# Kernel optimization log

Measured on AMD Instinct MI355X. Metric: run time of the kernel, lower is better.

The kernel has to match this reference:

```python
import jax, jax.numpy as jnp
import numpy as np

B = 128
IN = 256
NLVL = 6
KLVL = 3
CH = 4
C = 4 * CH * CH          # 64 channels per node
OU = 8                   # out_filter_siz_u
OV = 8                   # out_filter_siz_v
NK = 2 ** KLVL           # 8 leaf nodes per axis
W_SCALE = 1.0 / 16.0     # ~1/sqrt(2*2*C) so 7 stacked relu-convs stay numerically sane


def setup_inputs() -> dict:
    key = jax.random.key(0)
    ks = jax.random.split(key, 2 * NLVL + 4)
    fx = IN // 2 ** NLVL  # 4: input patch filter size
    inp = {}
    inp["in_data"] = jax.random.normal(ks[0], (B, IN, IN, 1), jnp.float32)
    inp["in_filter"] = jax.random.normal(ks[1], (fx, fx, 1, C), jnp.float32) * W_SCALE
    inp["in_bias"] = jnp.zeros((C,), jnp.float32)
    i = 2
    for lvl in range(1, NLVL + 1):
        n = 2 ** min(lvl, KLVL)  # node grid: grows to 2^klvl then stays
        inp[f"f{lvl}"] = jax.random.normal(ks[i], (n, n, 2, 2, C, C), jnp.float32) * W_SCALE
        inp[f"b{lvl}"] = jnp.zeros((n, n, C), jnp.float32)
        i += 1
    inp["Wd"] = jax.random.normal(ks[i], (NK, NK, 2, C, OU * OV), jnp.float32) * W_SCALE
    return inp


def _node_conv(x, w, b):
    # x: [Nu,Nv,B,H,W,C]; w: [Nu,Nv,2,2,C,C]; 2x2 stride-2 VALID conv per node
    Nu, Nv, Bn, H, W, Cc = x.shape
    xr = x.reshape(Nu, Nv, Bn, H // 2, 2, W // 2, 2, Cc)
    y = jnp.einsum('uvbhxwyc,uvxyco->uvbhwo', xr, w)
    return jax.nn.relu(y + b[:, :, None, None, None, :])


def _forward(in_data, in_filter, in_bias, fs, bs, Wd):
    Bn = in_data.shape[0]
    fx, fy = in_filter.shape[0], in_filter.shape[1]
    # input interp conv: stride == kernel -> non-overlapping patch GEMM
    xr = in_data[..., 0].reshape(Bn, in_data.shape[1] // fx, fx, in_data.shape[2] // fy, fy)
    x = jax.nn.relu(jnp.einsum('bxpyq,pqc->bxyc', xr, in_filter[:, :, 0, :]) + in_bias)
    x = x[None, None]  # [1,1,B,2^nlvl,2^nlvl,C] node grid
    for lvl in range(1, NLVL + 1):
        if lvl <= KLVL:
            # children (itu,itv) read parent (itu//2, itv//2)
            x = jnp.repeat(jnp.repeat(x, 2, axis=0), 2, axis=1)
        x = _node_conv(x, fs[lvl - 1], bs[lvl - 1])
    feats = x[:, :, :, 0, 0, :]  # [NK,NK,B,C]; spatial is 1x1 at level nlvl
    out = jnp.einsum('uvbc,uvrck->uvbrk', feats, Wd)  # r in {real, imag}
    out = out.reshape(NK, NK, Bn, 2, OU, OV)
    out = jnp.transpose(out, (2, 0, 4, 1, 5, 3))  # [B,itu,ou,itv,ov,2]
    return out.reshape(Bn, NK * OU, NK * OV, 2)


def reference(in_data, in_filter, in_bias, f1, b1, f2, b2, f3, b3, f4, b4, f5, b5, f6, b6, Wd):
    fs = (f1, f2, f3, f4, f5, f6)
    bs = (b1, b2, b3, b4, b5, b6)
    return _forward(in_data, in_filter, in_bias, fs, bs, Wd)
```

## Files before the change

### kernel.cpp

```cpp
#include <hip/hip_runtime.h>
#include <hip/hip_bf16.h>
#include <cstdint>
#include <cstddef>


typedef __attribute__((ext_vector_type(8))) short short8;
typedef __attribute__((ext_vector_type(4))) float f32x4;
typedef unsigned short ushort_t;

static __device__ __forceinline__ float b2f(const __hip_bfloat16 x) {
    return __bfloat162float(x);
}
static __device__ __forceinline__ ushort_t f2bf(float x) {
    __hip_bfloat16 h = __float2bfloat16(x);
    ushort_t u;
    __builtin_memcpy(&u, &h, 2);
    return u;
}
static __device__ __forceinline__ void gl_lds16(const void* g, void* l) {
    __builtin_amdgcn_global_load_lds(
        (const __attribute__((address_space(1))) void*)g,
        (__attribute__((address_space(3))) void*)l, 16, 0, 0);
}
#define WAIT_LGKM0() __builtin_amdgcn_s_waitcnt(0xC07F)
#define WAIT_VM0()   __builtin_amdgcn_s_waitcnt(0x0F70)

#define PREP_BLOCKS 2533

static __device__ __forceinline__ void prep_work(
    int gid, int isbf,
    const void* f1, const void* f2, const void* f3,
    const void* f4, const void* f5, const void* f6, const void* wdsrc,
    const void* b1, const void* b2, const void* b3,
    const void* b4, const void* b5, const void* b6,
    ushort_t* __restrict__ wbuf, ushort_t* __restrict__ wdbuf,
    float* __restrict__ bbuf)
{
    if (gid >= 648448) return;
    if (gid >= 630784) {
        const int bg = gid - 630784;
        const void* src; int base;
        if      (bg <   256) { src = b1; base = 0;     }
        else if (bg <  1280) { src = b2; base = 256;   }
        else if (bg <  5376) { src = b3; base = 1280;  }
        else if (bg <  9472) { src = b4; base = 5376;  }
        else if (bg < 13568) { src = b5; base = 9472;  }
        else                 { src = b6; base = 13568; }
        const int local = bg - base;
        bbuf[bg] = isbf ? b2f(((const __hip_bfloat16*)src)[local])
                        : ((const float*)src)[local];
        return;
    }
    if (gid >= 565248) {
        const int local = gid - 565248;
        const int lane = local & 63;
        const int slot = (local >> 6) & 15;
        const int site = local >> 10;
        const int ks2 = slot >> 3, nh = slot & 7, q = lane >> 4;
        const int n = nh * 16 + (lane & 15);
        const int r = n >> 6, kk = n & 63;
        const int cbase = ks2 * 32 + q * 8;
        ushort_t pk[8];
        if (isbf) {
            const ushort_t* s = (const ushort_t*)wdsrc;
            #pragma unroll
            for (int j = 0; j < 8; j++)
                pk[j] = s[(((size_t)(site * 2 + r) * 64 + cbase + j) * 64) + kk];
        } else {
            const float* s = (const float*)wdsrc;
            #pragma unroll
            for (int j = 0; j < 8; j++)
                pk[j] = f2bf(s[(((size_t)(site * 2 + r) * 64 + cbase + j) * 64) + kk]);
        }
        *(uint4*)&wdbuf[(size_t)local * 8] = *(uint4*)pk;
        return;
    }
    const void* fsrc; int base;
    if      (gid <   8192) { fsrc = f1; base = 0;      }
    else if (gid <  40960) { fsrc = f2; base = 8192;   }
    else if (gid < 172032) { fsrc = f3; base = 40960;  }
    else if (gid < 303104) { fsrc = f4; base = 172032; }
    else if (gid < 434176) { fsrc = f5; base = 303104; }
    else                   { fsrc = f6; base = 434176; }
    const int local = gid - base;
    const int lane = local & 63;
    const int slot = (local >> 6) & 7;
    const int sitetap = local >> 9;
    const int ks = slot >> 2, nh = slot & 3, q = lane >> 4;
    const int n = (lane & 15) + nh * 16;
    const int kbase = ks * 32 + q * 8;
    ushort_t pk[8];
    if (isbf) {
        const ushort_t* s = (const ushort_t*)fsrc + (size_t)sitetap * 4096;
        #pragma unroll
        for (int j = 0; j < 8; j++) pk[j] = s[(kbase + j) * 64 + n];
    } else {
        const float* s = (const float*)fsrc + (size_t)sitetap * 4096;
        #pragma unroll
        for (int j = 0; j < 8; j++) pk[j] = f2bf(s[(kbase + j) * 64 + n]);
    }
    *(uint4*)&wbuf[(size_t)gid * 8] = *(uint4*)pk;
}

static __device__ __forceinline__ void stage0_body(
    int blk, int isbf,
    const void* __restrict__ in_data, const void* __restrict__ filt,
    const void* __restrict__ bias, __hip_bfloat16* __restrict__ x0,
    int b_off)
{
    const int X  = blk & 63;
    const int bl = blk >> 6;
    const int bg = bl + b_off;

    __shared__ float sIn[4][256];
    __shared__ float sF[16][64];
    __shared__ float sB[64];

    const int t = threadIdx.x;
    const size_t srow = ((size_t)bg * 256 + (size_t)X * 4) * 256;

    if (isbf) {
        const __hip_bfloat16* src = (const __hip_bfloat16*)in_data + srow;
        #pragma unroll
        for (int i = 0; i < 4; i++) {
            int flat = i * 256 + t;
            int p = flat >> 8, col = flat & 255;
            sIn[p][col] = b2f(src[(size_t)p * 256 + col]);
        }
        const __hip_bfloat16* fsrc = (const __hip_bfloat16*)filt;
        #pragma unroll
        for (int i = 0; i < 4; i++) {
            int flat = i * 256 + t;
            sF[flat >> 6][flat & 63] = b2f(fsrc[flat]);
        }
        if (t < 64) sB[t] = b2f(((const __hip_bfloat16*)bias)[t]);
    } else {
        const float* src = (const float*)in_data + srow;
        const int p = t >> 6, c4 = (t & 63) * 4;
        *(float4*)&sIn[p][c4] = *(const float4*)(src + (size_t)p * 256 + c4);
        const float* fsrc = (const float*)filt;
        #pragma unroll
        for (int i = 0; i < 4; i++) {
            int flat = i * 256 + t;
            sF[flat >> 6][flat & 63] = fsrc[flat];
        }
        if (t < 64) sB[t] = ((const float*)bias)[t];
    }
    __syncthreads();

    const int ty = t >> 4;
    const int tc = t & 15;

    float acc[4][4];
    {
        const float4 bv = *(const float4*)&sB[tc * 4];
        #pragma unroll
        for (int yi = 0; yi < 4; yi++) {
            acc[yi][0] = bv.x; acc[yi][1] = bv.y;
            acc[yi][2] = bv.z; acc[yi][3] = bv.w;
        }
    }

    #pragma unroll
    for (int p = 0; p < 4; p++) {
        float4 rin[4], rf[4];
        #pragma unroll
        for (int yi = 0; yi < 4; yi++)
            rin[yi] = *(const float4*)&sIn[p][ty * 16 + yi * 4];
        #pragma unroll
        for (int q = 0; q < 4; q++)
            rf[q] = *(const float4*)&sF[p * 4 + q][tc * 4];
        #pragma unroll
        for (int yi = 0; yi < 4; yi++) {
            #pragma unroll
            for (int q = 0; q < 4; q++) {
                const float a = ((const float*)&rin[yi])[q];
                acc[yi][0] = fmaf(a, rf[q].x, acc[yi][0]);
                acc[yi][1] = fmaf(a, rf[q].y, acc[yi][1]);
                acc[yi][2] = fmaf(a, rf[q].z, acc[yi][2]);
                acc[yi][3] = fmaf(a, rf[q].w, acc[yi][3]);
            }
        }
    }

    ushort_t* dst = (ushort_t*)(x0 + ((size_t)bl * 64 + X) * 64 * 64);
    #pragma unroll
    for (int yi = 0; yi < 4; yi++) {
        uint2 pk;
        pk.x = (uint32_t)f2bf(fmaxf(acc[yi][0], 0.f))
             | ((uint32_t)f2bf(fmaxf(acc[yi][1], 0.f)) << 16);
        pk.y = (uint32_t)f2bf(fmaxf(acc[yi][2], 0.f))
             | ((uint32_t)f2bf(fmaxf(acc[yi][3], 0.f)) << 16);
        *(uint2*)(dst + (size_t)(ty * 4 + yi) * 64 + tc * 4) = pk;
    }
}

__global__ __launch_bounds__(256) void k_prep0(
    const void* __restrict__ in_data,
    const void* f1, const void* f2, const void* f3,
    const void* f4, const void* f5, const void* f6, const void* wdsrc,
    const void* b1, const void* b2, const void* b3,
    const void* b4, const void* b5, const void* b6,
    ushort_t* __restrict__ wbuf, ushort_t* __restrict__ wdbuf,
    float* __restrict__ bbuf, int* __restrict__ flag,
    const void* __restrict__ filt, const void* __restrict__ bias0,
    __hip_bfloat16* __restrict__ x0)
{
    __shared__ int sflag;
    const int t = threadIdx.x;
    if (t < 64) {
        const float v = __uint_as_float(((const uint32_t*)in_data)[t]);
        const bool plaus = (v == 0.0f) || (fabsf(v) > 1e-8f && fabsf(v) < 1e4f);
        const unsigned long long m = __ballot(plaus);
        if (t == 0) sflag = (__popcll(m) >= 48) ? 0 : 1;
    }
    __syncthreads();
    const int isbf = sflag;

    if (blockIdx.x < PREP_BLOCKS) {
        if (blockIdx.x == 0 && t == 0) *flag = isbf;
        prep_work(blockIdx.x * 256 + t, isbf,
                  f1, f2, f3, f4, f5, f6, wdsrc,
                  b1, b2, b3, b4, b5, b6, wbuf, wdbuf, bbuf);
    } else {
        stage0_body(blockIdx.x - PREP_BLOCKS, isbf, in_data, filt, bias0, x0, 0);
    }
}

__global__ __launch_bounds__(256) void k_stage0(
    const void* __restrict__ in_data, const void* __restrict__ filt,
    const void* __restrict__ bias, __hip_bfloat16* __restrict__ x0,
    const int* __restrict__ flag, int b_off)
{
    stage0_body(blockIdx.x, *flag, in_data, filt, bias, x0, b_off);
}

__global__ __launch_bounds__(256) void k_level4(
    const __hip_bfloat16* __restrict__ xin,
    const ushort_t* __restrict__ wbuf,
    const float* __restrict__ bbuf,
    __hip_bfloat16* __restrict__ xout,
    int Nv_out, int HW, int Bc, int mtiles)
{
    __shared__ ushort_t smem[20480];
    __shared__ float sBias[4][64];
    ushort_t* sA = smem;
    ushort_t* sB = smem + 4096;

    int idx = blockIdx.x;
    const int mt = idx % mtiles; idx /= mtiles;
    const int w  = idx % HW; idx /= HW;
    const int h  = idx % HW; idx /= HW;
    const int Nv_in = Nv_out >> 1;
    const int vp = idx % Nv_in;
    const int up = idx / Nv_in;

    const int t = threadIdx.x;
    const int wave = t >> 6, lane = t & 63;
    const int lm = lane & 15, lq = lane >> 4;

    {
        const int ct = t >> 6, o = t & 63;
        const int so_t = (2 * up + (ct >> 1)) * Nv_out + (2 * vp + (ct & 1));
        sBias[ct][o] = bbuf[so_t * 64 + o];
    }

    const int so = (2 * up + (wave >> 1)) * Nv_out + (2 * vp + (wave & 1));
    const int H_in = HW * 2;
    const size_t bstride = (size_t)H_in * H_in * 64;
    const size_t siteb = (size_t)(up * Nv_in + vp) * Bc * bstride;
    const ushort_t* wsite = wbuf + (size_t)so * 4 * 4096;

    const f32x4 zero = {0.f, 0.f, 0.f, 0.f};
    f32x4 acc[4][4];
    #pragma unroll
    for (int i = 0; i < 4; i++)
        #pragma unroll
        for (int j = 0; j < 4; j++) acc[i][j] = zero;

    for (int tap = 0; tap < 4; tap++) {
        const int hi = 2 * h + (tap >> 1), wi = 2 * w + (tap & 1);
        const size_t tapoff = siteb + ((size_t)hi * H_in + wi) * 64;
        #pragma unroll
        for (int s2 = 0; s2 < 2; s2++) {
            const int s = wave * 2 + s2;
            const int ks = s >> 2, mh = s & 3;
            int b = mt * 64 + lm + mh * 16;
            if (b >= Bc) b = Bc - 1;
            gl_lds16(xin + tapoff + (size_t)b * bstride + ks * 32 + lq * 8,
                     &sA[s * 512]);
        }
        const ushort_t* wt = wsite + (size_t)tap * 4096;
        #pragma unroll
        for (int s = 0; s < 8; s++) {
            gl_lds16(wt + s * 512 + lane * 8, &sB[wave * 4096 + s * 512]);
        }
        __syncthreads();

        #pragma unroll
        for (int ks = 0; ks < 2; ks++) {
            short8 bf0 = *(const short8*)&sB[wave * 4096 + (ks * 4 + 0) * 512 + lane * 8];
            short8 bf1 = *(const short8*)&sB[wave * 4096 + (ks * 4 + 1) * 512 + lane * 8];
            short8 bf2 = *(const short8*)&sB[wave * 4096 + (ks * 4 + 2) * 512 + lane * 8];
            short8 bf3 = *(const short8*)&sB[wave * 4096 + (ks * 4 + 3) * 512 + lane * 8];
            #pragma unroll
            for (int fm = 0; fm < 4; fm++) {
                short8 a = *(const short8*)&sA[(ks * 4 + fm) * 512 + lane * 8];
                acc[fm][0] = __builtin_amdgcn_mfma_f32_16x16x32_bf16(a, bf0, acc[fm][0], 0, 0, 0);
                acc[fm][1] = __builtin_amdgcn_mfma_f32_16x16x32_bf16(a, bf1, acc[fm][1], 0, 0, 0);
                acc[fm][2] = __builtin_amdgcn_mfma_f32_16x16x32_bf16(a, bf2, acc[fm][2], 0, 0, 0);
                acc[fm][3] = __builtin_amdgcn_mfma_f32_16x16x32_bf16(a, bf3, acc[fm][3], 0, 0, 0);
            }
        }
        __syncthreads();
    }

    float bv[4];
    #pragma unroll
    for (int fn = 0; fn < 4; fn++) bv[fn] = sBias[wave][fn * 16 + lm];
    ushort_t* so_buf = smem + wave * 4352;
    #pragma unroll
    for (int fm = 0; fm < 4; fm++) {
        #pragma unroll
        for (int fn = 0; fn < 4; fn++) {
            #pragma unroll
            for (int r = 0; r < 4; r++) {
                const int row = fm * 16 + lq * 4 + r;
                so_buf[row * 68 + fn * 16 + lm] =
                    f2bf(fmaxf(acc[fm][fn][r] + bv[fn], 0.f));
            }
        }
    }
    __syncthreads();

    const size_t ostride = (size_t)HW * HW * 64;
    const size_t obase = (size_t)so * Bc * ostride + ((size_t)h * HW + w) * 64;
    #pragma unroll
    for (int i = 0; i < 8; i++) {
        const int task = i * 64 + lane;
        const int oct = task & 7, row = task >> 3;
        const int b = mt * 64 + row;
        if (b < Bc) {
            *(uint4*)(xout + obase + (size_t)b * ostride + oct * 8) =
                *(const uint4*)&so_buf[row * 68 + oct * 8];
        }
    }
}

__global__ __launch_bounds__(256) void k_f456(
    const __hip_bfloat16* __restrict__ xin,
    const ushort_t* __restrict__ w4, const ushort_t* __restrict__ w5,
    const ushort_t* __restrict__ w6, const ushort_t* __restrict__ wd,
    const float* __restrict__ b4, const float* __restrict__ b5,
    const float* __restrict__ b6,
    void* __restrict__ out, const int* __restrict__ flag,
    int Bc, int b_off, int mtiles)
{
    const int isbf = *flag;
    const int bx = blockIdx.x;
    const int mt = bx % mtiles;
    const int site = bx / mtiles;
    const int u = site >> 3, v = site & 7;

    __shared__ ushort_t smem[37376];

    const int t = threadIdx.x;
    const int wv = t >> 6, lane = t & 63;
    const int lm = lane & 15, lq = lane >> 4;

    const ushort_t* w6s = w6 + (size_t)site * 16384 + lane * 8;
    const ushort_t* wds = wd + (size_t)site * 8192  + lane * 8;

    float bv4[4], bv5[4];
    #pragma unroll
    for (int fn = 0; fn < 4; fn++) {
        bv4[fn] = b4[site * 64 + fn * 16 + lm];
        bv5[fn] = b5[site * 64 + fn * 16 + lm];
    }
    const float bv6 = b6[site * 64 + wv * 16 + lm];

    {
        const ushort_t* w4s = w4 + (size_t)site * 16384;
        #pragma unroll
        for (int s2 = 0; s2 < 8; s2++) {
            const int s = wv * 8 + s2;
            gl_lds16(w4s + s * 512 + lane * 8, &smem[s * 512]);
        }
    }
    __syncthreads();

    const f32x4 zero = {0.f, 0.f, 0.f, 0.f};
    const int h5 = wv >> 1, w5p = wv & 1;
    ushort_t* mid1w = smem + 16384 + wv * 4224;
    ushort_t* Aw = smem + 33280 + wv * 1024;
    const size_t sb = (size_t)site * Bc;

    int brow = mt * 16 + lm;
    if (brow >= Bc) brow = Bc - 1;
    const __hip_bfloat16* xbase = xin + (sb + brow) * 4096 + lq * 8;

    for (int i = 0; i < 4; i++) {
        const int h4 = 2 * h5 + (i >> 1), w4p = 2 * w5p + (i & 1);
        f32x4 acc[4];
        #pragma unroll
        for (int b_ = 0; b_ < 4; b_++) acc[b_] = zero;

        for (int tap = 0; tap < 4; tap++) {
            const int h3 = 2 * h4 + (tap >> 1), w3 = 2 * w4p + (tap & 1);
            const int poff = (h3 * 8 + w3) * 64;
            WAIT_LGKM0();
            #pragma unroll
            for (int ks = 0; ks < 2; ks++) {
                gl_lds16(xbase + poff + ks * 32, &Aw[ks * 512]);
            }
            WAIT_VM0();
            __builtin_amdgcn_sched_barrier(0);
            #pragma unroll
            for (int ks = 0; ks < 2; ks++) {
                short8 a = *(const short8*)&Aw[ks * 512 + lane * 8];
                #pragma unroll
                for (int fn = 0; fn < 4; fn++) {
                    short8 bfr = *(const short8*)&smem[(tap * 8 + ks * 4 + fn) * 512 + lane * 8];
                    acc[fn] = __builtin_amdgcn_mfma_f32_16x16x32_bf16(a, bfr, acc[fn], 0, 0, 0);
                }
            }
        }
        #pragma unroll
        for (int fn = 0; fn < 4; fn++) {
            #pragma unroll
            for (int r = 0; r < 4; r++) {
                const int m = lq * 4 + r;
                const int ch = fn * 16 + lm;
                mid1w[m * 264 + i * 64 + ch] =
                    f2bf(fmaxf(acc[fn][r] + bv4[fn], 0.f));
            }
        }
    }
    __syncthreads();

    {
        const ushort_t* w5s = w5 + (size_t)site * 16384;
        #pragma unroll
        for (int s2 = 0; s2 < 8; s2++) {
            const int s = wv * 8 + s2;
            gl_lds16(w5s + s * 512 + lane * 8, &smem[s * 512]);
        }
    }
    __syncthreads();

    short8 b3r[8];
    short8 wdr[4];
    {
        f32x4 acc2[4];
        #pragma unroll
        for (int b_ = 0; b_ < 4; b_++) acc2[b_] = zero;

        #pragma unroll
        for (int i = 0; i < 4; i++) {
            #pragma unroll
            for (int ks = 0; ks < 2; ks++) {
                short8 a0 = *(const short8*)&mid1w[lm * 264 + i * 64 + ks * 32 + lq * 8];
                #pragma unroll
                for (int fn = 0; fn < 4; fn++) {
                    short8 bfr = *(const short8*)&smem[(i * 8 + ks * 4 + fn) * 512 + lane * 8];
                    acc2[fn] = __builtin_amdgcn_mfma_f32_16x16x32_bf16(a0, bfr, acc2[fn], 0, 0, 0);
                }
            }
        }

        #pragma unroll
        for (int tap = 0; tap < 4; tap++)
            #pragma unroll
            for (int ks = 0; ks < 2; ks++)
                b3r[tap * 2 + ks] = *(const short8*)(w6s + (tap * 8 + ks * 4 + wv) * 512);
        #pragma unroll
        for (int ks = 0; ks < 2; ks++)
            #pragma unroll
            for (int n2 = 0; n2 < 2; n2++)
                wdr[ks * 2 + n2] = *(const short8*)(wds + (ks * 8 + 2 * wv + n2) * 512);

        #pragma unroll
        for (int fn = 0; fn < 4; fn++) {
            #pragma unroll
            for (int r = 0; r < 4; r++) {
                const int m = lq * 4 + r;
                const int ch = fn * 16 + lm;
                mid1w[m * 72 + ch] =
                    f2bf(fmaxf(acc2[fn][r] + bv5[fn], 0.f));
            }
        }
    }
    __syncthreads();

    {
        f32x4 acc3 = zero;
        #pragma unroll
        for (int tap = 0; tap < 4; tap++) {
            const ushort_t* sl = smem + 16384 + tap * 4224;
            #pragma unroll
            for (int ks = 0; ks < 2; ks++) {
                short8 a0 = *(const short8*)&sl[lm * 72 + ks * 32 + lq * 8];
                acc3 = __builtin_amdgcn_mfma_f32_16x16x32_bf16(a0, b3r[tap * 2 + ks], acc3, 0, 0, 0);
            }
        }
        ushort_t* mid3 = smem + 33280;
        #pragma unroll
        for (int r = 0; r < 4; r++) {
            const int m = lq * 4 + r;
            const int ch = wv * 16 + lm;
            mid3[m * 72 + ch] = f2bf(fmaxf(acc3[r] + bv6, 0.f));
        }
    }
    __syncthreads();

    {
        const ushort_t* mid3 = smem + 33280;
        f32x4 acc4[2];
        acc4[0] = zero; acc4[1] = zero;
        #pragma unroll
        for (int ks = 0; ks < 2; ks++) {
            short8 a0 = *(const short8*)&mid3[lm * 72 + ks * 32 + lq * 8];
            #pragma unroll
            for (int n2 = 0; n2 < 2; n2++) {
                acc4[n2] = __builtin_amdgcn_mfma_f32_16x16x32_bf16(a0, wdr[ks * 2 + n2], acc4[n2], 0, 0, 0);
            }
        }
        #pragma unroll
        for (int n2 = 0; n2 < 2; n2++) {
            const int n = (2 * wv + n2) * 16 + lm;
            const int rr = n >> 6, ou = (n >> 3) & 7, ov = n & 7;
            const size_t obase =
                (((size_t)(u * 8 + ou)) * 64 + (v * 8 + ov)) * 2 + rr;
            #pragma unroll
            for (int reg = 0; reg < 4; reg++) {
                const int brw = mt * 16 + lq * 4 + reg;
                if (brw < Bc) {
                    const size_t oidx = obase + (size_t)(b_off + brw) * 8192;
                    if (isbf) ((__hip_bfloat16*)out)[oidx] =
                        __float2bfloat16(acc4[n2][reg]);
                    else ((float*)out)[oidx] = acc4[n2][reg];
                }
            }
        }
    }
}

extern "C" void kernel_launch(void* const* d_in, const int* in_sizes, int n_in,
                              void* d_out, int out_size, void* d_ws, size_t ws_size,
                              hipStream_t stream)
{
    (void)in_sizes; (void)n_in; (void)out_size;

    const void* in_data = d_in[0];
    const void* filt    = d_in[1];
    const void* bias0   = d_in[2];
    const void* fl[7];
    const void* bl[7];
    for (int l = 1; l <= 6; l++) {
        fl[l] = d_in[1 + 2 * l];
        bl[l] = d_in[2 + 2 * l];
    }
    const void* Wd = d_in[15];

    const int Bfull = 128;
    const size_t perB = (size_t)64 * 64 * 64;

    const size_t wbufBytes  = 565248ull * 16;
    const size_t wdbufBytes = 65536ull * 16;
    const size_t bbufBytes  = 17664ull * 4;
    const size_t headBytes  = 256 + wbufBytes + wdbufBytes + bbufBytes;

    const size_t avail = ws_size > headBytes ? ws_size - headBytes : 0;
    int Bc = 0;
    for (int c = 128; c >= 1; c >>= 1) {
        if ((size_t)2 * c * perB * sizeof(__hip_bfloat16) <= avail) { Bc = c; break; }
    }
    if (Bc == 0) return;

    int* flag = (int*)d_ws;
    ushort_t* wbuf  = (ushort_t*)((char*)d_ws + 256);
    ushort_t* wdbuf = (ushort_t*)((char*)d_ws + 256 + wbufBytes);
    float* bbuf = (float*)((char*)d_ws + 256 + wbufBytes + wdbufBytes);
    __hip_bfloat16* bufA = (__hip_bfloat16*)((char*)d_ws + headBytes);
    __hip_bfloat16* bufB = bufA + (size_t)Bc * perB;

    static const size_t w_off[7] = {0, 0, 65536, 327680, 1376256, 2424832, 3473408};
    static const int    b_off_tab[7] = {0, 0, 256, 1280, 5376, 9472, 13568};

    const int mt4 = (Bc + 63) / 64;
    const int mt16 = (Bc + 15) / 16;

    for (int b_off = 0; b_off < Bfull; b_off += Bc) {
        if (b_off == 0) {
            k_prep0<<<dim3(PREP_BLOCKS + Bc * 64), 256, 0, stream>>>(
                in_data,
                fl[1], fl[2], fl[3], fl[4], fl[5], fl[6], Wd,
                bl[1], bl[2], bl[3], bl[4], bl[5], bl[6],
                wbuf, wdbuf, bbuf, flag,
                filt, bias0, bufA);
        } else {
            k_stage0<<<dim3(Bc * 64), 256, 0, stream>>>(in_data, filt, bias0, bufA, flag, b_off);
        }

        __hip_bfloat16* cur = bufA;
        __hip_bfloat16* nxt = bufB;
        for (int lvl = 1; lvl <= 3; lvl++) {
            const int Nu = 1 << lvl;
            const int H  = 64 >> lvl;
            const int Nv_in = Nu >> 1;
            dim3 grid(Nv_in * Nv_in * H * H * mt4);
            k_level4<<<grid, 256, 0, stream>>>(cur, wbuf + w_off[lvl],
                bbuf + b_off_tab[lvl], nxt, Nu, H, Bc, mt4);
            __hip_bfloat16* tmp = cur; cur = nxt; nxt = tmp;
        }

        k_f456<<<dim3(64 * mt16), 256, 0, stream>>>(cur,
            wbuf + w_off[4], wbuf + w_off[5], wbuf + w_off[6], wdbuf,
            bbuf + b_off_tab[4], bbuf + b_off_tab[5], bbuf + b_off_tab[6],
            d_out, flag, Bc, b_off, mt16);
    }
}
```

Measured before the change: 249.6 us.

## Store activations position-major with batch innermost for contiguous per-tap loads

```diff
diff --git a/kernel.cpp b/kernel.cpp
--- a/kernel.cpp
+++ b/kernel.cpp
@@ -106,7 +106,7 @@
     int blk, int isbf,
     const void* __restrict__ in_data, const void* __restrict__ filt,
     const void* __restrict__ bias, __hip_bfloat16* __restrict__ x0,
-    int b_off)
+    int b_off, int Bc)
 {
     const int X  = blk & 63;
     const int bl = blk >> 6;
@@ -183,7 +183,7 @@
         }
     }
 
-    ushort_t* dst = (ushort_t*)(x0 + ((size_t)bl * 64 + X) * 64 * 64);
+    ushort_t* dst = (ushort_t*)x0;
     #pragma unroll
     for (int yi = 0; yi < 4; yi++) {
         uint2 pk;
@@ -191,7 +191,8 @@
              | ((uint32_t)f2bf(fmaxf(acc[yi][1], 0.f)) << 16);
         pk.y = (uint32_t)f2bf(fmaxf(acc[yi][2], 0.f))
              | ((uint32_t)f2bf(fmaxf(acc[yi][3], 0.f)) << 16);
-        *(uint2*)(dst + (size_t)(ty * 4 + yi) * 64 + tc * 4) = pk;
+        const int wpos = ty * 4 + yi;
+        *(uint2*)(dst + ((size_t)(X * 64 + wpos) * Bc + bl) * 64 + tc * 4) = pk;
     }
 }
 
@@ -204,7 +205,7 @@
     ushort_t* __restrict__ wbuf, ushort_t* __restrict__ wdbuf,
     float* __restrict__ bbuf, int* __restrict__ flag,
     const void* __restrict__ filt, const void* __restrict__ bias0,
-    __hip_bfloat16* __restrict__ x0)
+    __hip_bfloat16* __restrict__ x0, int Bc)
 {
     __shared__ int sflag;
     const int t = threadIdx.x;
@@ -223,16 +224,16 @@
                   f1, f2, f3, f4, f5, f6, wdsrc,
                   b1, b2, b3, b4, b5, b6, wbuf, wdbuf, bbuf);
     } else {
-        stage0_body(blockIdx.x - PREP_BLOCKS, isbf, in_data, filt, bias0, x0, 0);
+        stage0_body(blockIdx.x - PREP_BLOCKS, isbf, in_data, filt, bias0, x0, 0, Bc);
     }
 }
 
 __global__ __launch_bounds__(256) void k_stage0(
     const void* __restrict__ in_data, const void* __restrict__ filt,
     const void* __restrict__ bias, __hip_bfloat16* __restrict__ x0,
-    const int* __restrict__ flag, int b_off)
+    const int* __restrict__ flag, int b_off, int Bc)
 {
-    stage0_body(blockIdx.x, *flag, in_data, filt, bias, x0, b_off);
+    stage0_body(blockIdx.x, *flag, in_data, filt, bias, x0, b_off, Bc);
 }
 
 __global__ __launch_bounds__(256) void k_level4(
@@ -267,8 +268,8 @@
 
     const int so = (2 * up + (wave >> 1)) * Nv_out + (2 * vp + (wave & 1));
     const int H_in = HW * 2;
-    const size_t bstride = (size_t)H_in * H_in * 64;
-    const size_t siteb = (size_t)(up * Nv_in + vp) * Bc * bstride;
+    const size_t pstride = (size_t)Bc * 64;
+    const size_t siteb = (size_t)(up * Nv_in + vp) * H_in * H_in * pstride;
     const ushort_t* wsite = wbuf + (size_t)so * 4 * 4096;
 
     const f32x4 zero = {0.f, 0.f, 0.f, 0.f};
@@ -280,14 +281,14 @@
 
     for (int tap = 0; tap < 4; tap++) {
         const int hi = 2 * h + (tap >> 1), wi = 2 * w + (tap & 1);
-        const size_t tapoff = siteb + ((size_t)hi * H_in + wi) * 64;
+        const size_t tapoff = siteb + ((size_t)hi * H_in + wi) * pstride;
         #pragma unroll
         for (int s2 = 0; s2 < 2; s2++) {
             const int s = wave * 2 + s2;
             const int ks = s >> 2, mh = s & 3;
             int b = mt * 64 + lm + mh * 16;
             if (b >= Bc) b = Bc - 1;
-            gl_lds16(xin + tapoff + (size_t)b * bstride + ks * 32 + lq * 8,
+            gl_lds16(xin + tapoff + (size_t)b * 64 + ks * 32 + lq * 8,
                      &sA[s * 512]);
         }
         const ushort_t* wt = wsite + (size_t)tap * 4096;
@@ -333,15 +334,14 @@
     }
     __syncthreads();
 
-    const size_t ostride = (size_t)HW * HW * 64;
-    const size_t obase = (size_t)so * Bc * ostride + ((size_t)h * HW + w) * 64;
+    const size_t obase = ((size_t)so * HW * HW + (size_t)h * HW + w) * pstride;
     #pragma unroll
     for (int i = 0; i < 8; i++) {
         const int task = i * 64 + lane;
         const int oct = task & 7, row = task >> 3;
         const int b = mt * 64 + row;
         if (b < Bc) {
-            *(uint4*)(xout + obase + (size_t)b * ostride + oct * 8) =
+            *(uint4*)(xout + obase + (size_t)b * 64 + oct * 8) =
                 *(const uint4*)&so_buf[row * 68 + oct * 8];
         }
     }
@@ -393,11 +393,12 @@
     const int h5 = wv >> 1, w5p = wv & 1;
     ushort_t* mid1w = smem + 16384 + wv * 4224;
     ushort_t* Aw = smem + 33280 + wv * 1024;
-    const size_t sb = (size_t)site * Bc;
+    const size_t pstride = (size_t)Bc * 64;
 
     int brow = mt * 16 + lm;
     if (brow >= Bc) brow = Bc - 1;
-    const __hip_bfloat16* xbase = xin + (sb + brow) * 4096 + lq * 8;
+    const __hip_bfloat16* xbase =
+        xin + (size_t)site * 64 * pstride + (size_t)brow * 64 + lq * 8;
 
     for (int i = 0; i < 4; i++) {
         const int h4 = 2 * h5 + (i >> 1), w4p = 2 * w5p + (i & 1);
@@ -407,7 +408,7 @@
 
         for (int tap = 0; tap < 4; tap++) {
             const int h3 = 2 * h4 + (tap >> 1), w3 = 2 * w4p + (tap & 1);
-            const int poff = (h3 * 8 + w3) * 64;
+            const size_t poff = (size_t)(h3 * 8 + w3) * pstride;
             WAIT_LGKM0();
             #pragma unroll
             for (int ks = 0; ks < 2; ks++) {
@@ -597,9 +598,9 @@
                 fl[1], fl[2], fl[3], fl[4], fl[5], fl[6], Wd,
                 bl[1], bl[2], bl[3], bl[4], bl[5], bl[6],
                 wbuf, wdbuf, bbuf, flag,
-                filt, bias0, bufA);
+                filt, bias0, bufA, Bc);
         } else {
-            k_stage0<<<dim3(Bc * 64), 256, 0, stream>>>(in_data, filt, bias0, bufA, flag, b_off);
+            k_stage0<<<dim3(Bc * 64), 256, 0, stream>>>(in_data, filt, bias0, bufA, flag, b_off, Bc);
         }
 
         __hip_bfloat16* cur = bufA;
```

Result: no change. 249.0 us (-0.2%).
